# Kernel optimization log

Measured on AMD Instinct MI355X. Metric: run time of the kernel, lower is better.

Reference implementation:

```python
import jax, jax.numpy as jnp
import numpy as np

C, S, K, SIGMA = 512, 11, 3, 16
B = 128
EPS = 1e-5  # BatchNorm eps (eval mode, running_mean=0, running_var=1)


def _make_dct_weight(Cc, H, W):
    # FcaNet 'low16' frequency selection
    lx = [0, 0, 1, 1, 0, 2, 2, 1, 2, 0, 3, 4, 0, 1, 3, 0]
    ly = [0, 1, 0, 1, 2, 0, 1, 2, 2, 3, 0, 0, 4, 3, 1, 5]
    mx = [u * (H // 7) for u in lx]
    my = [v * (W // 7) for v in ly]
    w = np.zeros((Cc, H, W), np.float32)
    cp = Cc // len(lx)

    def bf(pos, freq, POS):
        r = np.cos(np.pi * freq * (pos + 0.5) / POS) / np.sqrt(POS)
        return r if freq == 0 else r * np.sqrt(2.0)

    for i, (u, v) in enumerate(zip(mx, my)):
        for tx in range(H):
            for ty in range(W):
                w[i * cp:(i + 1) * cp, tx, ty] = bf(tx, u, H) * bf(ty, v, W)
    return jnp.asarray(w)


def _bn(f, g, b):
    # eval-mode BatchNorm2d: (f - 0)/sqrt(1+eps)*g + b, per channel (axis 1)
    s = g / jnp.sqrt(1.0 + EPS)
    return f * s[None, :, None, None] + b[None, :, None, None]


def _conv1x1(f, w, b):
    return jnp.einsum('bchw,oc->bohw', f, w) + b[None, :, None, None]


def _spatial_kernel(f, w_conv, b_conv, g_sp, b_sp):
    Bn = f.shape[0]
    s = _conv1x1(f, w_conv, b_conv)                  # (B, K*K, S, S)
    s = s.reshape(Bn, K * K, S * S).transpose(0, 2, 1)  # (B, S*S, K*K)
    s = _bn(s.reshape(Bn, S * S, K, K), g_sp, b_sp)
    return s.reshape(Bn, S * S, K * K)


def _channel_kernel(f, dct_w, fc1, fc2, g_ch, b_ch):
    y = jnp.sum(f * dct_w[None], axis=(-2, -1))      # (B, C) DCT pooling
    y = jax.nn.sigmoid(jax.nn.relu(y @ fc1.T) @ fc2.T)  # (B, C*K*K)
    y = _bn(y.reshape(-1, C, K, K), g_ch, b_ch)
    return y.reshape(-1, C, K * K)


def _unfold(f):
    # torch-style per-pixel kxk neighborhoods -> (B, C, H, W, K, K)
    p = (K + 1) // 2 - 1
    Bn, Cn, H, W = f.shape
    fp = jnp.pad(f, ((0, 0), (0, 0), (p, p), (p, p)))
    pat = jnp.stack([fp[:, :, di:di + H, dj:dj + W]
                     for di in range(K) for dj in range(K)], axis=-1)
    return pat.reshape(Bn, Cn, H, W, K, K)


def setup_inputs() -> dict:
    key = jax.random.key(0)
    ks = iter(jax.random.split(key, 32))

    def nrm(shape, s=0.02):
        return s * jax.random.normal(next(ks), shape, jnp.float32)

    def gma(shape):
        return 1.0 + 0.1 * jax.random.normal(next(ks), shape, jnp.float32)

    return dict(
        x=jax.random.normal(next(ks), (B, C, S, S), jnp.float32),
        dct_w=_make_dct_weight(C, S, S),
        w_conv=nrm((K * K, C)), b_conv=nrm((K * K,)),
        g_sp=gma((S * S,)), b_sp=nrm((S * S,), 0.05),
        g_ch=gma((C,)), b_ch=nrm((C,), 0.05),
        fc1=nrm((C // SIGMA, C)), fc2=nrm((C * K * K, C // SIGMA)),
        up_w1=nrm((2 * C, C)), up_b1=nrm((2 * C,)), up_g1=gma((2 * C,)), up_bb1=nrm((2 * C,), 0.05),
        up_w2=nrm((2 * C, 2 * C)), up_b2=nrm((2 * C,)), up_g2=gma((2 * C,)), up_bb2=nrm((2 * C,), 0.05),
        lo_w1=nrm((2 * C, 2 * C)), lo_b1=nrm((2 * C,)), lo_g1=gma((2 * C,)), lo_bb1=nrm((2 * C,), 0.05),
        lo_w2=nrm((C, 2 * C)), lo_b2=nrm((C,)), lo_g2=gma((C,)), lo_bb2=nrm((C,), 0.05),
    )


def reference(x, dct_w, w_conv, b_conv, g_sp, b_sp, g_ch, b_ch, fc1, fc2,
              up_w1, up_b1, up_g1, up_bb1, up_w2, up_b2, up_g2, up_bb2,
              lo_w1, lo_b1, lo_g1, lo_bb1, lo_w2, lo_b2, lo_g2, lo_bb2):
    Bn = x.shape[0]
    # instance kernel: spatial (B,1,HW,KK) x channel (B,C,1,KK)
    sk = _spatial_kernel(x, w_conv, b_conv, g_sp, b_sp)[:, None]
    ck = _channel_kernel(x, dct_w, fc1, fc2, g_ch, b_ch)[:, :, None]
    inst = (sk * ck).reshape(Bn, C, S, S, K, K)
    # CLM task representation (sum over batch between upper and lower)
    a = jax.nn.relu(_bn(_conv1x1(x, up_w1, up_b1), up_g1, up_bb1))
    a = jax.nn.relu(_bn(_conv1x1(a, up_w2, up_b2), up_g2, up_bb2))
    a = a.sum(axis=0, keepdims=True)
    a = jax.nn.relu(_bn(_conv1x1(a, lo_w1, lo_b1), lo_g1, lo_bb1))
    task_s = jax.nn.sigmoid(_bn(_conv1x1(a, lo_w2, lo_b2), lo_g2, lo_bb2))
    # task kernel (shared across the batch)
    sk_t = _spatial_kernel(task_s, w_conv, b_conv, g_sp, b_sp)[:, None]
    ck_t = _channel_kernel(task_s, dct_w, fc1, fc2, g_ch, b_ch)[:, :, None]
    task_kernel = (sk_t * ck_t).reshape(1, C, S, S, K, K)
    kernel = task_kernel * inst
    adapted = (_unfold(x) * kernel).mean(axis=(-1, -2))  # (B,C,S,S)
    return adapted + x, task_kernel
```

## Files before the change

kernel.cpp:

```cpp
#include <hip/hip_runtime.h>
#include <hip/hip_bf16.h>
#include <math.h>

#define BNEPS 1e-5f
#define BDIM_B 128
#define CDIM 512
#define SS 121
#define KK 9
#define MROWS (BDIM_B * SS)

typedef unsigned short u16;
typedef __bf16 bf16x8 __attribute__((ext_vector_type(8)));
typedef float f32x4 __attribute__((ext_vector_type(4)));

__device__ __forceinline__ u16 f2bf(float f) {
    union { float f; unsigned int u; } v; v.f = f;
    unsigned int r = v.u + 0x7FFF + ((v.u >> 16) & 1);
    return (u16)(r >> 16);
}
__device__ __forceinline__ float bf2f(u16 v) {
    union { unsigned int u; float f; } x; x.u = ((unsigned int)v) << 16; return x.f;
}

__device__ __forceinline__ void gld16(const u16* g, u16* l) {
    __builtin_amdgcn_global_load_lds(
        (const __attribute__((address_space(1))) void*)g,
        (__attribute__((address_space(3))) void*)l, 16, 0, 0);
}

template<int MODE, int SWIZ>
__global__ __launch_bounds__(256)
void gemm_mfma(const u16* __restrict__ A, const u16* __restrict__ Bw,
               const float* __restrict__ bias, const float* __restrict__ g,
               const float* __restrict__ bb, void* __restrict__ out,
               int Kd, int N, int NT)
{
    __shared__ __align__(16) u16 Als[2][128 * 32];
    __shared__ __align__(16) u16 Bls[2][128 * 32];

    const int tid  = threadIdx.x;
    const int lane = tid & 63;
    const int w    = tid >> 6;
    const int wm   = w >> 1, wn = w & 1;

    int bx, by;
    if (SWIZ) {
        int i = blockIdx.x;
        if (i < 960) {
            int xg = i & 7;
            int j  = i >> 3;
            bx = xg * 15 + (j >> 3);
            by = j & 7;
        } else { bx = 120; by = i - 960; }
    } else {
        bx = blockIdx.x / NT; by = blockIdx.x - bx * NT;
    }
    const int bm = bx * 128;
    const int bn = by * 128;

    f32x4 acc[4][4] = {};

    const int subrow = tid >> 2;
    const int kq     = tid & 3;
    const int gchunk = kq ^ ((subrow >> 1) & 3);
    const u16* Ab = A  + (size_t)(bm + subrow) * Kd + gchunk * 8;
    const u16* Bb = Bw + (size_t)(bn + subrow) * Kd + gchunk * 8;
    u16* Al0  = &Als[0][(w * 16) * 32];
    u16* Al1  = &Als[0][(w * 16 + 64) * 32];
    u16* Bl0  = &Bls[0][(w * 16) * 32];
    u16* Bl1  = &Bls[0][(w * 16 + 64) * 32];
    u16* Al0b = &Als[1][(w * 16) * 32];
    u16* Al1b = &Als[1][(w * 16 + 64) * 32];
    u16* Bl0b = &Bls[1][(w * 16) * 32];
    u16* Bl1b = &Bls[1][(w * 16 + 64) * 32];

    const int fa_row = wm * 64 + (lane & 15);
    const int fb_row = wn * 64 + (lane & 15);
    const int kofs   = (((lane >> 4) ^ (((lane & 15) >> 1) & 3))) * 8;

    for (int k0 = 0; k0 < Kd; k0 += 64) {
        __syncthreads();
        gld16(Ab + k0,                      Al0);
        gld16(Ab + (size_t)64 * Kd + k0,    Al1);
        gld16(Bb + k0,                      Bl0);
        gld16(Bb + (size_t)64 * Kd + k0,    Bl1);
        gld16(Ab + k0 + 32,                 Al0b);
        gld16(Ab + (size_t)64 * Kd + k0 + 32, Al1b);
        gld16(Bb + k0 + 32,                 Bl0b);
        gld16(Bb + (size_t)64 * Kd + k0 + 32, Bl1b);
        __syncthreads();

        #pragma unroll
        for (int hb = 0; hb < 2; ++hb) {
            const u16* Ah = &Als[hb][0];
            const u16* Bh = &Bls[hb][0];
            bf16x8 af[4], bfv[4];
            #pragma unroll
            for (int i = 0; i < 4; ++i)
                af[i] = *(const bf16x8*)&Ah[(fa_row + i * 16) * 32 + kofs];
            #pragma unroll
            for (int j = 0; j < 4; ++j)
                bfv[j] = *(const bf16x8*)&Bh[(fb_row + j * 16) * 32 + kofs];
            #pragma unroll
            for (int i = 0; i < 4; ++i)
                #pragma unroll
                for (int j = 0; j < 4; ++j)
                    acc[i][j] = __builtin_amdgcn_mfma_f32_16x16x32_bf16(af[i], bfv[j], acc[i][j], 0, 0, 0);
        }
    }

    const float inv = 1.0f / sqrtf(1.0f + BNEPS);

    if (MODE == 1) {
        u16* Y = (u16*)out;
        int dstrow[4][4];
        #pragma unroll
        for (int i = 0; i < 4; ++i) {
            int mb = bm + wm * 64 + i * 16 + (lane >> 4) * 4;
            #pragma unroll
            for (int r = 0; r < 4; ++r) {
                int m = mb + r;
                int b = m / 121, p = m - b * 121;
                dstrow[i][r] = p * 128 + b;
            }
        }
        #pragma unroll
        for (int j = 0; j < 4; ++j) {
            int n = bn + wn * 64 + j * 16 + (lane & 15);
            float sc = g[n] * inv, bo = bias[n], bv = bb[n];
            #pragma unroll
            for (int i = 0; i < 4; ++i)
                #pragma unroll
                for (int r = 0; r < 4; ++r) {
                    float v = (acc[i][j][r] + bo) * sc + bv;
                    v = fmaxf(v, 0.0f);
                    Y[(size_t)dstrow[i][r] * N + n] = f2bf(v);
                }
        }
    } else if (MODE == 2) {
        float ps[4];
        #pragma unroll
        for (int j = 0; j < 4; ++j) {
            int n = bn + wn * 64 + j * 16 + (lane & 15);
            float sc = g[n] * inv, bo = bias[n], bv = bb[n];
            float s = 0.f;
            #pragma unroll
            for (int i = 0; i < 4; ++i)
                #pragma unroll
                for (int r = 0; r < 4; ++r) {
                    float v = (acc[i][j][r] + bo) * sc + bv;
                    s += fmaxf(v, 0.0f);
                }
            ps[j] = s;
        }
        __syncthreads();
        float* red = (float*)Als;
        #pragma unroll
        for (int j = 0; j < 4; ++j)
            red[(wm * 4 + (lane >> 4)) * 128 + wn * 64 + j * 16 + (lane & 15)] = ps[j];
        __syncthreads();
        if (tid < 128) {
            float s = 0.f;
            #pragma unroll
            for (int r = 0; r < 8; ++r) s += red[r * 128 + tid];
            ((u16*)out)[(size_t)bx * N + bn + tid] = f2bf(s);
        }
    } else {
        u16* Y = (u16*)out;
        #pragma unroll
        for (int j = 0; j < 4; ++j) {
            int n = bn + wn * 64 + j * 16 + (lane & 15);
            float sc = g[n] * inv, bo = bias[n], bv = bb[n];
            #pragma unroll
            for (int i = 0; i < 4; ++i) {
                int mb = bm + wm * 64 + i * 16 + (lane >> 4) * 4;
                #pragma unroll
                for (int r = 0; r < 4; ++r) {
                    float v = (acc[i][j][r] + bo) * sc + bv;
                    if (MODE == 3) v = fmaxf(v, 0.0f);
                    else           v = 1.f / (1.f + expf(-v));
                    Y[(size_t)(mb + r) * N + n] = f2bf(v);
                }
            }
        }
    }
}

#define W1N (1024 * 512)
#define W2N (1024 * 1024)
#define L1N (1024 * 1024)
#define L2N (512 * 1024)
#define DCTN (512 * 121)
#define WCN (16 * 512)
#define PREP_ELEM (W1N + W2N + L1N + L2N + DCTN + WCN)
#define PREP_BLKS (1024 + (PREP_ELEM + 255) / 256)
__global__ void prep_combo(const float* __restrict__ x, u16* __restrict__ Xb,
                           const float* __restrict__ w1, const float* __restrict__ w2,
                           const float* __restrict__ l1, const float* __restrict__ l2,
                           const float* __restrict__ dct, const float* __restrict__ w_conv,
                           u16* __restrict__ o1, u16* __restrict__ o2,
                           u16* __restrict__ o3, u16* __restrict__ o4,
                           float* __restrict__ dctT, u16* __restrict__ wcb)
{
    __shared__ float t[64 * 121];
    if (blockIdx.x < 1024) {
        int b = blockIdx.x >> 3, c0 = (blockIdx.x & 7) * 64;
        for (int idx = threadIdx.x; idx < 64 * 121; idx += 256) {
            int c = idx / 121, p = idx - c * 121;
            t[idx] = x[((size_t)b * 512 + c0 + c) * 121 + p];
        }
        __syncthreads();
        for (int idx = threadIdx.x; idx < 121 * 64; idx += 256) {
            int p = idx >> 6, c = idx & 63;
            Xb[((size_t)(b * 121 + p)) * 512 + c0 + c] = f2bf(t[c * 121 + p]);
        }
        return;
    }
    int i = (blockIdx.x - 1024) * 256 + threadIdx.x;
    if (i < W1N) { o1[i] = f2bf(w1[i]); return; }
    i -= W1N;
    if (i < W2N) { o2[i] = f2bf(w2[i]); return; }
    i -= W2N;
    if (i < L1N) { o3[i] = f2bf(l1[i]); return; }
    i -= L1N;
    if (i < L2N) { o4[i] = f2bf(l2[i]); return; }
    i -= L2N;
    if (i < DCTN) {
        int p = i >> 9, c = i & 511;
        dctT[i] = dct[(size_t)c * 121 + p];
        return;
    }
    i -= DCTN;
    if (i < WCN) {
        int n = i >> 9, c = i & 511;
        wcb[i] = (n < 9) ? f2bf(w_conv[(size_t)n * 512 + c]) : (u16)0;
    }
}

__global__ __launch_bounds__(256)
void spatial_ck_combo(const u16* __restrict__ Xb, const u16* __restrict__ Xt,
                      const u16* __restrict__ wcb, const float* __restrict__ b_conv,
                      const float* __restrict__ g_sp, const float* __restrict__ b_sp,
                      const float* __restrict__ dctT,
                      const float* __restrict__ fc1, const float* __restrict__ fc2,
                      const float* __restrict__ g_ch, const float* __restrict__ b_ch,
                      float* __restrict__ skb, float* __restrict__ skt,
                      float* __restrict__ ckbuf, float* __restrict__ ck_t)
{
    const float inv = 1.0f / sqrtf(1.0f + BNEPS);

    if (blockIdx.x < 122) {
        const int tid  = threadIdx.x;
        const int lane = tid & 63;
        const int w    = tid >> 6;
        const bool task = (blockIdx.x == 121);
        const u16* Arow = task ? Xt : Xb + (size_t)blockIdx.x * 128 * 512;

        const int fr = lane & 15;
        const int kq = lane >> 4;
        const int r0 = w * 32;

        f32x4 acc0 = {}, acc1 = {};
        const u16* a0p = Arow + (size_t)(r0 + fr) * 512 + kq * 8;
        const u16* a1p = Arow + (size_t)(r0 + 16 + fr) * 512 + kq * 8;
        const u16* bp  = wcb + (size_t)fr * 512 + kq * 8;
        #pragma unroll
        for (int k0 = 0; k0 < 512; k0 += 32) {
            bf16x8 a0 = *(const bf16x8*)(a0p + k0);
            bf16x8 a1 = *(const bf16x8*)(a1p + k0);
            bf16x8 b  = *(const bf16x8*)(bp + k0);
            acc0 = __builtin_amdgcn_mfma_f32_16x16x32_bf16(a0, b, acc0, 0, 0, 0);
            acc1 = __builtin_amdgcn_mfma_f32_16x16x32_bf16(a1, b, acc1, 0, 0, 0);
        }

        int n = lane & 15;
        if (n < 9) {
            float bo = b_conv[n];
            #pragma unroll
            for (int t = 0; t < 2; ++t) {
                f32x4 a = t ? acc1 : acc0;
                #pragma unroll
                for (int r = 0; r < 4; ++r) {
                    int mloc = r0 + t * 16 + (lane >> 4) * 4 + r;
                    if (!task) {
                        int m = blockIdx.x * 128 + mloc;
                        int p = m % 121;
                        float v = (a[r] + bo) * (g_sp[p] * inv) + b_sp[p];
                        skb[(size_t)m * 9 + n] = v;
                    } else if (mloc < 121) {
                        float v = (a[r] + bo) * (g_sp[mloc] * inv) + b_sp[mloc];
                        skt[(size_t)mloc * 9 + n] = v;
                    }
                }
            }
        }
        return;
    }

    __shared__ float yls[512];
    __shared__ float y2ls[32];
    const int g = blockIdx.x - 122;
    const u16* src = (g < 128) ? Xb + (size_t)g * 121 * 512 : Xt;

    for (int c = threadIdx.x; c < 512; c += 256) {
        float s = 0.f;
        for (int p = 0; p < SS; ++p)
            s += bf2f(src[(size_t)p * 512 + c]) * dctT[p * 512 + c];
        yls[c] = s;
    }
    __syncthreads();

    {
        int o = threadIdx.x >> 3, kp = threadIdx.x & 7;
        const float* w = fc1 + (size_t)o * 512;
        float s = 0.f;
        for (int k = kp * 4; k < 512; k += 32) {
            float4 wv = *(const float4*)(w + k);
            float4 av = *(const float4*)(yls + k);
            s += wv.x * av.x + wv.y * av.y + wv.z * av.z + wv.w * av.w;
        }
        s += __shfl_xor(s, 1);
        s += __shfl_xor(s, 2);
        s += __shfl_xor(s, 4);
        if (kp == 0) y2ls[o] = fmaxf(s, 0.f);
    }
    __syncthreads();

    for (int o = threadIdx.x; o < CDIM * KK; o += 256) {
        const float* w = fc2 + (size_t)o * 32;
        float s = 0.f;
        #pragma unroll
        for (int k = 0; k < 32; ++k) s += y2ls[k] * w[k];
        s = 1.f / (1.f + expf(-s));
        int c = o / KK;
        s = s * (g_ch[c] * inv) + b_ch[c];
        if (g < 128) ckbuf[(size_t)g * CDIM * KK + o] = s;
        else         ck_t[o] = s;
    }
}

#define TKN (CDIM * SS * KK)
#define FIN_BLKS (1024 + (TKN + 255) / 256)
__global__ __launch_bounds__(256)
void final_combo(const float* __restrict__ x, const float* __restrict__ skb,
                 const float* __restrict__ sk_t, const float* __restrict__ ckbuf,
                 const float* __restrict__ ck_t, float* __restrict__ out0,
                 float* __restrict__ tk)
{
    __shared__ float PS[SS * KK];
    __shared__ float CS[64 * KK];
    __shared__ float XT[64 * SS];

    if (blockIdx.x >= 1024) {
        int idx = (blockIdx.x - 1024) * 256 + threadIdx.x;
        if (idx < TKN) {
            int k9 = idx % KK;
            int pc = idx / KK;
            int p = pc % SS, c = pc / SS;
            tk[idx] = sk_t[p * KK + k9] * ck_t[c * KK + k9];
        }
        return;
    }

    const int tid = threadIdx.x;
    const int b = blockIdx.x >> 3, c0 = (blockIdx.x & 7) * 64;

    const float* sp = skb + (size_t)b * SS * KK;
    for (int i = tid; i < SS * KK; i += 256) PS[i] = sp[i] * sk_t[i];
    const float* cp = ckbuf + ((size_t)b * CDIM + c0) * KK;
    const float* tp = ck_t + (size_t)c0 * KK;
    for (int i = tid; i < 64 * KK; i += 256) CS[i] = cp[i] * tp[i];
    const float* xp = x + ((size_t)b * CDIM + c0) * SS;
    for (int i = tid; i < 64 * SS; i += 256) XT[i] = xp[i];
    __syncthreads();

    float* op = out0 + ((size_t)b * CDIM + c0) * SS;
    for (int i = tid; i < 64 * SS; i += 256) {
        int c = i / SS, p = i - c * SS;
        int h = p / 11, w = p - h * 11;
        const float* xc = XT + c * SS;
        const float* ps = PS + p * KK;
        const float* cs = CS + c * KK;
        float acc = 0.f;
        #pragma unroll
        for (int di = 0; di < 3; ++di) {
            int hh = h + di - 1;
            bool hv = (unsigned)hh < 11u;
            #pragma unroll
            for (int dj = 0; dj < 3; ++dj) {
                int ww = w + dj - 1;
                int k = di * 3 + dj;
                float xv = (hv && (unsigned)ww < 11u) ? xc[hh * 11 + ww] : 0.f;
                acc += xv * ps[k] * cs[k];
            }
        }
        op[i] = acc * (1.0f / 9.0f) + xc[p];
    }
}

extern "C" void kernel_launch(void* const* d_in, const int* in_sizes, int n_in,
                              void* d_out, int out_size, void* d_ws, size_t ws_size,
                              hipStream_t stream)
{
    const float* x      = (const float*)d_in[0];
    const float* dct_w  = (const float*)d_in[1];
    const float* w_conv = (const float*)d_in[2];
    const float* b_conv = (const float*)d_in[3];
    const float* g_sp   = (const float*)d_in[4];
    const float* b_sp   = (const float*)d_in[5];
    const float* g_ch   = (const float*)d_in[6];
    const float* b_ch   = (const float*)d_in[7];
    const float* fc1    = (const float*)d_in[8];
    const float* fc2    = (const float*)d_in[9];
    const float* up_w1  = (const float*)d_in[10];
    const float* up_b1  = (const float*)d_in[11];
    const float* up_g1  = (const float*)d_in[12];
    const float* up_bb1 = (const float*)d_in[13];
    const float* up_w2  = (const float*)d_in[14];
    const float* up_b2  = (const float*)d_in[15];
    const float* up_g2  = (const float*)d_in[16];
    const float* up_bb2 = (const float*)d_in[17];
    const float* lo_w1  = (const float*)d_in[18];
    const float* lo_b1  = (const float*)d_in[19];
    const float* lo_g1  = (const float*)d_in[20];
    const float* lo_bb1 = (const float*)d_in[21];
    const float* lo_w2  = (const float*)d_in[22];
    const float* lo_b2  = (const float*)d_in[23];
    const float* lo_g2  = (const float*)d_in[24];
    const float* lo_bb2 = (const float*)d_in[25];

    float* out0 = (float*)d_out;
    float* tk   = out0 + (size_t)BDIM_B * CDIM * SS;

    char* ws = (char*)d_ws;
    size_t off = 0;
    auto alloc = [&](size_t bytes) { void* p = ws + off; off += (bytes + 63) & ~(size_t)63; return p; };
    u16*   Xb      = (u16*)alloc((size_t)MROWS * 512 * 2);
    u16*   Y1      = (u16*)alloc((size_t)MROWS * 1024 * 2);
    u16*   w1b     = (u16*)alloc((size_t)W1N * 2);
    u16*   w2b     = (u16*)alloc((size_t)W2N * 2);
    u16*   lw1b    = (u16*)alloc((size_t)L1N * 2);
    u16*   lw2b    = (u16*)alloc((size_t)L2N * 2);
    u16*   asum_b  = (u16*)alloc((size_t)128 * 1024 * 2);
    u16*   a3b     = (u16*)alloc((size_t)128 * 1024 * 2);
    u16*   ts_pc   = (u16*)alloc((size_t)128 * 512 * 2);
    float* dctT    = (float*)alloc((size_t)SS * 512 * 4);
    u16*   wcb     = (u16*)alloc((size_t)WCN * 2);
    float* ckbuf   = (float*)alloc((size_t)BDIM_B * CDIM * KK * 4);
    float* skbuf   = (float*)alloc((size_t)BDIM_B * SS * KK * 4);
    float* ck_t    = (float*)alloc((size_t)CDIM * KK * 4);
    float* sk_t    = (float*)alloc((size_t)SS * KK * 4);

    hipLaunchKernelGGL(prep_combo, dim3(PREP_BLKS), dim3(256), 0, stream,
                       x, Xb, up_w1, up_w2, lo_w1, lo_w2, dct_w, w_conv,
                       w1b, w2b, lw1b, lw2b, dctT, wcb);

    hipLaunchKernelGGL((gemm_mfma<1, 1>), dim3(121 * 8), dim3(256), 0, stream,
                       Xb, w1b, up_b1, up_g1, up_bb1, (void*)Y1, 512, 1024, 8);
    hipLaunchKernelGGL((gemm_mfma<2, 1>), dim3(121 * 8), dim3(256), 0, stream,
                       Y1, w2b, up_b2, up_g2, up_bb2, (void*)asum_b, 1024, 1024, 8);

    hipLaunchKernelGGL((gemm_mfma<3, 0>), dim3(8), dim3(256), 0, stream,
                       asum_b, lw1b, lo_b1, lo_g1, lo_bb1, (void*)a3b, 1024, 1024, 8);
    hipLaunchKernelGGL((gemm_mfma<4, 0>), dim3(4), dim3(256), 0, stream,
                       a3b, lw2b, lo_b2, lo_g2, lo_bb2, (void*)ts_pc, 1024, 512, 4);

    hipLaunchKernelGGL(spatial_ck_combo, dim3(122 + 129), dim3(256), 0, stream,
                       Xb, ts_pc, wcb, b_conv, g_sp, b_sp,
                       dctT, fc1, fc2, g_ch, b_ch,
                       skbuf, sk_t, ckbuf, ck_t);

    hipLaunchKernelGGL(final_combo, dim3(FIN_BLKS), dim3(256), 0, stream,
                       x, skbuf, sk_t, ckbuf, ck_t, out0, tk);
}
```

Baseline: 318.3 us.

## Double-buffer GEMM K-loop, fuse small GEMMs with spatial/channel kernels, vectorize loads

The main MFMA GEMM loop now uses a double-buffered LDS scheme. It prefetches the next 32-wide K slice while computing the current one, with one barrier per step instead of two. The small lower-branch GEMMs move to a new direct-load MFMA kernel. The first of them is fused into one launch with the per-instance spatial and channel kernel work, and the task-kernel computation is split into its own tiny launch. Weight bf16 conversion, channel-kernel DCT pooling, and the final epilogue loads and stores are vectorized, trading some code complexity for fewer launches and better overlap.

```diff
diff --git a/kernel.cpp b/kernel.cpp
--- a/kernel.cpp
+++ b/kernel.cpp
@@ -65,49 +65,41 @@
     const int gchunk = kq ^ ((subrow >> 1) & 3);
     const u16* Ab = A  + (size_t)(bm + subrow) * Kd + gchunk * 8;
     const u16* Bb = Bw + (size_t)(bn + subrow) * Kd + gchunk * 8;
-    u16* Al0  = &Als[0][(w * 16) * 32];
-    u16* Al1  = &Als[0][(w * 16 + 64) * 32];
-    u16* Bl0  = &Bls[0][(w * 16) * 32];
-    u16* Bl1  = &Bls[0][(w * 16 + 64) * 32];
-    u16* Al0b = &Als[1][(w * 16) * 32];
-    u16* Al1b = &Als[1][(w * 16 + 64) * 32];
-    u16* Bl0b = &Bls[1][(w * 16) * 32];
-    u16* Bl1b = &Bls[1][(w * 16 + 64) * 32];
 
     const int fa_row = wm * 64 + (lane & 15);
     const int fb_row = wn * 64 + (lane & 15);
     const int kofs   = (((lane >> 4) ^ (((lane & 15) >> 1) & 3))) * 8;
 
-    for (int k0 = 0; k0 < Kd; k0 += 64) {
+    const int NK = Kd >> 5;
+
+#define STG(bf_, t_) do { \
+    gld16(Ab + (size_t)(t_) * 32,                 &Als[bf_][(w * 16) * 32]); \
+    gld16(Ab + (size_t)64 * Kd + (size_t)(t_) * 32, &Als[bf_][(w * 16 + 64) * 32]); \
+    gld16(Bb + (size_t)(t_) * 32,                 &Bls[bf_][(w * 16) * 32]); \
+    gld16(Bb + (size_t)64 * Kd + (size_t)(t_) * 32, &Bls[bf_][(w * 16 + 64) * 32]); \
+} while (0)
+
+    STG(0, 0);
+    __syncthreads();
+    int cur = 0;
+    for (int t = 0; t < NK; ++t) {
+        if (t + 1 < NK) STG(cur ^ 1, t + 1);
+        bf16x8 af[4], bfv[4];
+        #pragma unroll
+        for (int i = 0; i < 4; ++i)
+            af[i] = *(const bf16x8*)&Als[cur][(fa_row + i * 16) * 32 + kofs];
+        #pragma unroll
+        for (int j = 0; j < 4; ++j)
+            bfv[j] = *(const bf16x8*)&Bls[cur][(fb_row + j * 16) * 32 + kofs];
+        #pragma unroll
+        for (int i = 0; i < 4; ++i)
+            #pragma unroll
+            for (int j = 0; j < 4; ++j)
+                acc[i][j] = __builtin_amdgcn_mfma_f32_16x16x32_bf16(af[i], bfv[j], acc[i][j], 0, 0, 0);
         __syncthreads();
-        gld16(Ab + k0,                      Al0);
-        gld16(Ab + (size_t)64 * Kd + k0,    Al1);
-        gld16(Bb + k0,                      Bl0);
-        gld16(Bb + (size_t)64 * Kd + k0,    Bl1);
-        gld16(Ab + k0 + 32,                 Al0b);
-        gld16(Ab + (size_t)64 * Kd + k0 + 32, Al1b);
-        gld16(Bb + k0 + 32,                 Bl0b);
-        gld16(Bb + (size_t)64 * Kd + k0 + 32, Bl1b);
-        __syncthreads();
-
-        #pragma unroll
-        for (int hb = 0; hb < 2; ++hb) {
-            const u16* Ah = &Als[hb][0];
-            const u16* Bh = &Bls[hb][0];
-            bf16x8 af[4], bfv[4];
-            #pragma unroll
-            for (int i = 0; i < 4; ++i)
-                af[i] = *(const bf16x8*)&Ah[(fa_row + i * 16) * 32 + kofs];
-            #pragma unroll
-            for (int j = 0; j < 4; ++j)
-                bfv[j] = *(const bf16x8*)&Bh[(fb_row + j * 16) * 32 + kofs];
-            #pragma unroll
-            for (int i = 0; i < 4; ++i)
-                #pragma unroll
-                for (int j = 0; j < 4; ++j)
-                    acc[i][j] = __builtin_amdgcn_mfma_f32_16x16x32_bf16(af[i], bfv[j], acc[i][j], 0, 0, 0);
-        }
-    }
+        cur ^= 1;
+    }
+#undef STG
 
     const float inv = 1.0f / sqrtf(1.0f + BNEPS);
 
@@ -137,7 +129,7 @@
                     Y[(size_t)dstrow[i][r] * N + n] = f2bf(v);
                 }
         }
-    } else if (MODE == 2) {
+    } else {
         float ps[4];
         #pragma unroll
         for (int j = 0; j < 4; ++j) {
@@ -165,34 +157,217 @@
             for (int r = 0; r < 8; ++r) s += red[r * 128 + tid];
             ((u16*)out)[(size_t)bx * N + bn + tid] = f2bf(s);
         }
-    } else {
-        u16* Y = (u16*)out;
+    }
+}
+
+template<int MODE>
+__device__ __forceinline__ void gemm_small_body(
+    const u16* __restrict__ A, const u16* __restrict__ Bw,
+    const float* __restrict__ bias, const float* __restrict__ g,
+    const float* __restrict__ bb, u16* __restrict__ Y,
+    int Kd, int N, int bn)
+{
+    const int tid  = threadIdx.x;
+    const int lane = tid & 63;
+    const int w    = tid >> 6;
+    const int fr   = lane & 15;
+    const int kq   = lane >> 4;
+    const int r0   = w * 32;
+
+    f32x4 acc[2][4] = {};
+    const u16* a0p = A + (size_t)(r0 + fr) * Kd + kq * 8;
+    const u16* a1p = a0p + (size_t)16 * Kd;
+    const u16* bp  = Bw + (size_t)(bn + fr) * Kd + kq * 8;
+
+    #pragma unroll 4
+    for (int k0 = 0; k0 < Kd; k0 += 32) {
+        bf16x8 a0 = *(const bf16x8*)(a0p + k0);
+        bf16x8 a1 = *(const bf16x8*)(a1p + k0);
         #pragma unroll
         for (int j = 0; j < 4; ++j) {
-            int n = bn + wn * 64 + j * 16 + (lane & 15);
-            float sc = g[n] * inv, bo = bias[n], bv = bb[n];
-            #pragma unroll
-            for (int i = 0; i < 4; ++i) {
-                int mb = bm + wm * 64 + i * 16 + (lane >> 4) * 4;
-                #pragma unroll
-                for (int r = 0; r < 4; ++r) {
-                    float v = (acc[i][j][r] + bo) * sc + bv;
-                    if (MODE == 3) v = fmaxf(v, 0.0f);
-                    else           v = 1.f / (1.f + expf(-v));
-                    Y[(size_t)(mb + r) * N + n] = f2bf(v);
+            bf16x8 bv = *(const bf16x8*)(bp + (size_t)j * 16 * Kd + k0);
+            acc[0][j] = __builtin_amdgcn_mfma_f32_16x16x32_bf16(a0, bv, acc[0][j], 0, 0, 0);
+            acc[1][j] = __builtin_amdgcn_mfma_f32_16x16x32_bf16(a1, bv, acc[1][j], 0, 0, 0);
+        }
+    }
+
+    const float inv = 1.0f / sqrtf(1.0f + BNEPS);
+    #pragma unroll
+    for (int j = 0; j < 4; ++j) {
+        int n = bn + j * 16 + (lane & 15);
+        float sc = g[n] * inv, bo = bias[n], bv = bb[n];
+        #pragma unroll
+        for (int t = 0; t < 2; ++t)
+            #pragma unroll
+            for (int r = 0; r < 4; ++r) {
+                int m = r0 + t * 16 + (lane >> 4) * 4 + r;
+                float v = (acc[t][j][r] + bo) * sc + bv;
+                if (MODE == 3) v = fmaxf(v, 0.0f);
+                else           v = 1.f / (1.f + expf(-v));
+                Y[(size_t)m * N + n] = f2bf(v);
+            }
+    }
+}
+
+template<int MODE>
+__global__ __launch_bounds__(256)
+void gemm_small(const u16* __restrict__ A, const u16* __restrict__ Bw,
+                const float* __restrict__ bias, const float* __restrict__ g,
+                const float* __restrict__ bb, u16* __restrict__ Y,
+                int Kd, int N)
+{
+    gemm_small_body<MODE>(A, Bw, bias, g, bb, Y, Kd, N, blockIdx.x * 64);
+}
+
+__device__ __forceinline__ void spatial_body(
+    const u16* __restrict__ Arow, const u16* __restrict__ wcb,
+    const float* __restrict__ b_conv, const float* __restrict__ g_sp,
+    const float* __restrict__ b_sp, float* __restrict__ skb,
+    bool task, int blk, float* __restrict__ skt)
+{
+    const float inv = 1.0f / sqrtf(1.0f + BNEPS);
+    const int tid  = threadIdx.x;
+    const int lane = tid & 63;
+    const int w    = tid >> 6;
+    const int fr   = lane & 15;
+    const int kq   = lane >> 4;
+    const int r0   = w * 32;
+
+    f32x4 acc0 = {}, acc1 = {};
+    const u16* a0p = Arow + (size_t)(r0 + fr) * 512 + kq * 8;
+    const u16* a1p = a0p + (size_t)16 * 512;
+    const u16* bp  = wcb + (size_t)fr * 512 + kq * 8;
+    #pragma unroll
+    for (int k0 = 0; k0 < 512; k0 += 32) {
+        bf16x8 a0 = *(const bf16x8*)(a0p + k0);
+        bf16x8 a1 = *(const bf16x8*)(a1p + k0);
+        bf16x8 b  = *(const bf16x8*)(bp + k0);
+        acc0 = __builtin_amdgcn_mfma_f32_16x16x32_bf16(a0, b, acc0, 0, 0, 0);
+        acc1 = __builtin_amdgcn_mfma_f32_16x16x32_bf16(a1, b, acc1, 0, 0, 0);
+    }
+
+    int n = lane & 15;
+    if (n < 9) {
+        float bo = b_conv[n];
+        #pragma unroll
+        for (int t = 0; t < 2; ++t) {
+            f32x4 a = t ? acc1 : acc0;
+            #pragma unroll
+            for (int r = 0; r < 4; ++r) {
+                int mloc = r0 + t * 16 + (lane >> 4) * 4 + r;
+                if (!task) {
+                    int m = blk * 128 + mloc;
+                    int p = m % 121;
+                    float v = (a[r] + bo) * (g_sp[p] * inv) + b_sp[p];
+                    skb[(size_t)m * 9 + n] = v;
+                } else if (mloc < 121) {
+                    float v = (a[r] + bo) * (g_sp[mloc] * inv) + b_sp[mloc];
+                    skt[(size_t)mloc * 9 + n] = v;
                 }
             }
         }
     }
+}
+
+__device__ __forceinline__ void channel_body(
+    const u16* __restrict__ src, const float* __restrict__ dctT,
+    const float* __restrict__ fc1, const float* __restrict__ fc2,
+    const float* __restrict__ g_ch, const float* __restrict__ b_ch,
+    float* __restrict__ outp, float* yls, float* y2ls)
+{
+    const float inv = 1.0f / sqrtf(1.0f + BNEPS);
+
+    {
+        int c = threadIdx.x * 2;
+        float s0 = 0.f, s1 = 0.f;
+        for (int p = 0; p < SS; ++p) {
+            unsigned v = *(const unsigned*)(src + (size_t)p * 512 + c);
+            float2 d  = *(const float2*)(dctT + (size_t)p * 512 + c);
+            s0 += bf2f((u16)(v & 0xFFFFu)) * d.x;
+            s1 += bf2f((u16)(v >> 16)) * d.y;
+        }
+        yls[c] = s0; yls[c + 1] = s1;
+    }
+    __syncthreads();
+
+    {
+        int o = threadIdx.x >> 3, kp = threadIdx.x & 7;
+        const float* w = fc1 + (size_t)o * 512;
+        float s = 0.f;
+        for (int k = kp * 4; k < 512; k += 32) {
+            float4 wv = *(const float4*)(w + k);
+            float4 av = *(const float4*)(yls + k);
+            s += wv.x * av.x + wv.y * av.y + wv.z * av.z + wv.w * av.w;
+        }
+        s += __shfl_xor(s, 1);
+        s += __shfl_xor(s, 2);
+        s += __shfl_xor(s, 4);
+        if (kp == 0) y2ls[o] = fmaxf(s, 0.f);
+    }
+    __syncthreads();
+
+    for (int o = threadIdx.x; o < CDIM * KK; o += 256) {
+        const float* w = fc2 + (size_t)o * 32;
+        float s = 0.f;
+        #pragma unroll
+        for (int k = 0; k < 32; ++k) s += y2ls[k] * w[k];
+        s = 1.f / (1.f + expf(-s));
+        int c = o / KK;
+        s = s * (g_ch[c] * inv) + b_ch[c];
+        outp[o] = s;
+    }
+}
+
+__global__ __launch_bounds__(256)
+void lo1_spatial(const u16* __restrict__ asum_b, const u16* __restrict__ lw1b,
+                 const float* __restrict__ lo_b1, const float* __restrict__ lo_g1,
+                 const float* __restrict__ lo_bb1, u16* __restrict__ a3b,
+                 const u16* __restrict__ Xb, const u16* __restrict__ wcb,
+                 const float* __restrict__ b_conv, const float* __restrict__ g_sp,
+                 const float* __restrict__ b_sp, const float* __restrict__ dctT,
+                 const float* __restrict__ fc1, const float* __restrict__ fc2,
+                 const float* __restrict__ g_ch, const float* __restrict__ b_ch,
+                 float* __restrict__ skb, float* __restrict__ ckbuf)
+{
+    __shared__ float sm[544];
+    int bi = blockIdx.x;
+    if (bi < 16) {
+        gemm_small_body<3>(asum_b, lw1b, lo_b1, lo_g1, lo_bb1, a3b, 1024, 1024, bi * 64);
+        return;
+    }
+    bi -= 16;
+    if (bi < 121) {
+        spatial_body(Xb + (size_t)bi * 128 * 512, wcb, b_conv, g_sp, b_sp, skb, false, bi, nullptr);
+        return;
+    }
+    bi -= 121;
+    channel_body(Xb + (size_t)bi * 121 * 512, dctT, fc1, fc2, g_ch, b_ch,
+                 ckbuf + (size_t)bi * CDIM * KK, sm, sm + 512);
+}
+
+__global__ __launch_bounds__(256)
+void task_combo(const u16* __restrict__ ts_pc, const u16* __restrict__ wcb,
+                const float* __restrict__ b_conv, const float* __restrict__ g_sp,
+                const float* __restrict__ b_sp, const float* __restrict__ dctT,
+                const float* __restrict__ fc1, const float* __restrict__ fc2,
+                const float* __restrict__ g_ch, const float* __restrict__ b_ch,
+                float* __restrict__ skt, float* __restrict__ ck_t)
+{
+    __shared__ float sm[544];
+    if (blockIdx.x == 0)
+        spatial_body(ts_pc, wcb, b_conv, g_sp, b_sp, nullptr, true, 0, skt);
+    else
+        channel_body(ts_pc, dctT, fc1, fc2, g_ch, b_ch, ck_t, sm, sm + 512);
 }
 
 #define W1N (1024 * 512)
 #define W2N (1024 * 1024)
 #define L1N (1024 * 1024)
 #define L2N (512 * 1024)
+#define VECN ((W1N + W2N + L1N + L2N) / 4)
 #define DCTN (512 * 121)
 #define WCN (16 * 512)
-#define PREP_ELEM (W1N + W2N + L1N + L2N + DCTN + WCN)
+#define PREP_ELEM (VECN + DCTN + WCN)
 #define PREP_BLKS (1024 + (PREP_ELEM + 255) / 256)
 __global__ void prep_combo(const float* __restrict__ x, u16* __restrict__ Xb,
                            const float* __restrict__ w1, const float* __restrict__ w2,
@@ -217,14 +392,21 @@
         return;
     }
     int i = (blockIdx.x - 1024) * 256 + threadIdx.x;
-    if (i < W1N) { o1[i] = f2bf(w1[i]); return; }
-    i -= W1N;
-    if (i < W2N) { o2[i] = f2bf(w2[i]); return; }
-    i -= W2N;
-    if (i < L1N) { o3[i] = f2bf(l1[i]); return; }
-    i -= L1N;
-    if (i < L2N) { o4[i] = f2bf(l2[i]); return; }
-    i -= L2N;
+    if (i < VECN) {
+        int q = i;
+        const float* s; u16* d;
+        if (q < W1N / 4)                    { s = w1; d = o1; }
+        else if (q < (W1N + W2N) / 4)       { s = w2; d = o2; q -= W1N / 4; }
+        else if (q < (W1N + W2N + L1N) / 4) { s = l1; d = o3; q -= (W1N + W2N) / 4; }
+        else                                { s = l2; d = o4; q -= (W1N + W2N + L1N) / 4; }
+        float4 v = ((const float4*)s)[q];
+        uint2 r;
+        r.x = (unsigned)f2bf(v.x) | ((unsigned)f2bf(v.y) << 16);
+        r.y = (unsigned)f2bf(v.z) | ((unsigned)f2bf(v.w) << 16);
+        ((uint2*)d)[q] = r;
+        return;
+    }
+    i -= VECN;
     if (i < DCTN) {
         int p = i >> 9, c = i & 511;
         dctT[i] = dct[(size_t)c * 121 + p];
@@ -234,108 +416,6 @@
     if (i < WCN) {
         int n = i >> 9, c = i & 511;
         wcb[i] = (n < 9) ? f2bf(w_conv[(size_t)n * 512 + c]) : (u16)0;
-    }
-}
-
-__global__ __launch_bounds__(256)
-void spatial_ck_combo(const u16* __restrict__ Xb, const u16* __restrict__ Xt,
-                      const u16* __restrict__ wcb, const float* __restrict__ b_conv,
-                      const float* __restrict__ g_sp, const float* __restrict__ b_sp,
-                      const float* __restrict__ dctT,
-                      const float* __restrict__ fc1, const float* __restrict__ fc2,
-                      const float* __restrict__ g_ch, const float* __restrict__ b_ch,
-                      float* __restrict__ skb, float* __restrict__ skt,
-                      float* __restrict__ ckbuf, float* __restrict__ ck_t)
-{
-    const float inv = 1.0f / sqrtf(1.0f + BNEPS);
-
-    if (blockIdx.x < 122) {
-        const int tid  = threadIdx.x;
-        const int lane = tid & 63;
-        const int w    = tid >> 6;
-        const bool task = (blockIdx.x == 121);
-        const u16* Arow = task ? Xt : Xb + (size_t)blockIdx.x * 128 * 512;
-
-        const int fr = lane & 15;
-        const int kq = lane >> 4;
-        const int r0 = w * 32;
-
-        f32x4 acc0 = {}, acc1 = {};
-        const u16* a0p = Arow + (size_t)(r0 + fr) * 512 + kq * 8;
-        const u16* a1p = Arow + (size_t)(r0 + 16 + fr) * 512 + kq * 8;
-        const u16* bp  = wcb + (size_t)fr * 512 + kq * 8;
-        #pragma unroll
-        for (int k0 = 0; k0 < 512; k0 += 32) {
-            bf16x8 a0 = *(const bf16x8*)(a0p + k0);
-            bf16x8 a1 = *(const bf16x8*)(a1p + k0);
-            bf16x8 b  = *(const bf16x8*)(bp + k0);
-            acc0 = __builtin_amdgcn_mfma_f32_16x16x32_bf16(a0, b, acc0, 0, 0, 0);
-            acc1 = __builtin_amdgcn_mfma_f32_16x16x32_bf16(a1, b, acc1, 0, 0, 0);
-        }
-
-        int n = lane & 15;
-        if (n < 9) {
-            float bo = b_conv[n];
-            #pragma unroll
-            for (int t = 0; t < 2; ++t) {
-                f32x4 a = t ? acc1 : acc0;
-                #pragma unroll
-                for (int r = 0; r < 4; ++r) {
-                    int mloc = r0 + t * 16 + (lane >> 4) * 4 + r;
-                    if (!task) {
-                        int m = blockIdx.x * 128 + mloc;
-                        int p = m % 121;
-                        float v = (a[r] + bo) * (g_sp[p] * inv) + b_sp[p];
-                        skb[(size_t)m * 9 + n] = v;
-                    } else if (mloc < 121) {
-                        float v = (a[r] + bo) * (g_sp[mloc] * inv) + b_sp[mloc];
-                        skt[(size_t)mloc * 9 + n] = v;
-                    }
-                }
-            }
-        }
-        return;
-    }
-
-    __shared__ float yls[512];
-    __shared__ float y2ls[32];
-    const int g = blockIdx.x - 122;
-    const u16* src = (g < 128) ? Xb + (size_t)g * 121 * 512 : Xt;
-
-    for (int c = threadIdx.x; c < 512; c += 256) {
-        float s = 0.f;
-        for (int p = 0; p < SS; ++p)
-            s += bf2f(src[(size_t)p * 512 + c]) * dctT[p * 512 + c];
-        yls[c] = s;
-    }
-    __syncthreads();
-
-    {
-        int o = threadIdx.x >> 3, kp = threadIdx.x & 7;
-        const float* w = fc1 + (size_t)o * 512;
-        float s = 0.f;
-        for (int k = kp * 4; k < 512; k += 32) {
-            float4 wv = *(const float4*)(w + k);
-            float4 av = *(const float4*)(yls + k);
-            s += wv.x * av.x + wv.y * av.y + wv.z * av.z + wv.w * av.w;
-        }
-        s += __shfl_xor(s, 1);
-        s += __shfl_xor(s, 2);
-        s += __shfl_xor(s, 4);
-        if (kp == 0) y2ls[o] = fmaxf(s, 0.f);
-    }
-    __syncthreads();
-
-    for (int o = threadIdx.x; o < CDIM * KK; o += 256) {
-        const float* w = fc2 + (size_t)o * 32;
-        float s = 0.f;
-        #pragma unroll
-        for (int k = 0; k < 32; ++k) s += y2ls[k] * w[k];
-        s = 1.f / (1.f + expf(-s));
-        int c = o / KK;
-        s = s * (g_ch[c] * inv) + b_ch[c];
-        if (g < 128) ckbuf[(size_t)g * CDIM * KK + o] = s;
-        else         ck_t[o] = s;
     }
 }
 
@@ -369,32 +449,44 @@
     for (int i = tid; i < SS * KK; i += 256) PS[i] = sp[i] * sk_t[i];
     const float* cp = ckbuf + ((size_t)b * CDIM + c0) * KK;
     const float* tp = ck_t + (size_t)c0 * KK;
-    for (int i = tid; i < 64 * KK; i += 256) CS[i] = cp[i] * tp[i];
+    for (int i = tid; i < (64 * KK) / 4; i += 256) {
+        float4 a = ((const float4*)cp)[i];
+        float4 bq = ((const float4*)tp)[i];
+        float4 r; r.x = a.x * bq.x; r.y = a.y * bq.y; r.z = a.z * bq.z; r.w = a.w * bq.w;
+        ((float4*)CS)[i] = r;
+    }
     const float* xp = x + ((size_t)b * CDIM + c0) * SS;
-    for (int i = tid; i < 64 * SS; i += 256) XT[i] = xp[i];
+    for (int i = tid; i < (64 * SS) / 4; i += 256)
+        ((float4*)XT)[i] = ((const float4*)xp)[i];
     __syncthreads();
 
     float* op = out0 + ((size_t)b * CDIM + c0) * SS;
-    for (int i = tid; i < 64 * SS; i += 256) {
-        int c = i / SS, p = i - c * SS;
-        int h = p / 11, w = p - h * 11;
-        const float* xc = XT + c * SS;
-        const float* ps = PS + p * KK;
-        const float* cs = CS + c * KK;
-        float acc = 0.f;
-        #pragma unroll
-        for (int di = 0; di < 3; ++di) {
-            int hh = h + di - 1;
-            bool hv = (unsigned)hh < 11u;
-            #pragma unroll
-            for (int dj = 0; dj < 3; ++dj) {
-                int ww = w + dj - 1;
-                int k = di * 3 + dj;
-                float xv = (hv && (unsigned)ww < 11u) ? xc[hh * 11 + ww] : 0.f;
-                acc += xv * ps[k] * cs[k];
+    for (int ci = tid; ci < (64 * SS) / 4; ci += 256) {
+        float4 o;
+        #pragma unroll
+        for (int r = 0; r < 4; ++r) {
+            int i = ci * 4 + r;
+            int c = i / SS, p = i - c * SS;
+            int h = p / 11, w = p - h * 11;
+            const float* xc = XT + c * SS;
+            const float* ps = PS + p * KK;
+            const float* cs = CS + c * KK;
+            float acc = 0.f;
+            #pragma unroll
+            for (int di = 0; di < 3; ++di) {
+                int hh = h + di - 1;
+                bool hv = (unsigned)hh < 11u;
+                #pragma unroll
+                for (int dj = 0; dj < 3; ++dj) {
+                    int ww = w + dj - 1;
+                    int k = di * 3 + dj;
+                    float xv = (hv && (unsigned)ww < 11u) ? xc[hh * 11 + ww] : 0.f;
+                    acc += xv * ps[k] * cs[k];
+                }
             }
-        }
-        op[i] = acc * (1.0f / 9.0f) + xc[p];
+            ((float*)&o)[r] = acc * (1.0f / 9.0f) + xc[p];
+        }
+        ((float4*)op)[ci] = o;
     }
 }
 
@@ -460,15 +552,18 @@
     hipLaunchKernelGGL((gemm_mfma<2, 1>), dim3(121 * 8), dim3(256), 0, stream,
                        Y1, w2b, up_b2, up_g2, up_bb2, (void*)asum_b, 1024, 1024, 8);
 
-    hipLaunchKernelGGL((gemm_mfma<3, 0>), dim3(8), dim3(256), 0, stream,
-                       asum_b, lw1b, lo_b1, lo_g1, lo_bb1, (void*)a3b, 1024, 1024, 8);
-    hipLaunchKernelGGL((gemm_mfma<4, 0>), dim3(4), dim3(256), 0, stream,
-                       a3b, lw2b, lo_b2, lo_g2, lo_bb2, (void*)ts_pc, 1024, 512, 4);
-
-    hipLaunchKernelGGL(spatial_ck_combo, dim3(122 + 129), dim3(256), 0, stream,
-                       Xb, ts_pc, wcb, b_conv, g_sp, b_sp,
+    hipLaunchKernelGGL(lo1_spatial, dim3(16 + 121 + 128), dim3(256), 0, stream,
+                       asum_b, lw1b, lo_b1, lo_g1, lo_bb1, a3b,
+                       Xb, wcb, b_conv, g_sp, b_sp,
                        dctT, fc1, fc2, g_ch, b_ch,
-                       skbuf, sk_t, ckbuf, ck_t);
+                       skbuf, ckbuf);
+
+    hipLaunchKernelGGL((gemm_small<4>), dim3(8), dim3(256), 0, stream,
+                       a3b, lw2b, lo_b2, lo_g2, lo_bb2, ts_pc, 1024, 512);
+
+    hipLaunchKernelGGL(task_combo, dim3(2), dim3(256), 0, stream,
+                       ts_pc, wcb, b_conv, g_sp, b_sp,
+                       dctT, fc1, fc2, g_ch, b_ch, sk_t, ck_t);
 
     hipLaunchKernelGGL(final_combo, dim3(FIN_BLKS), dim3(256), 0, stream,
                        x, skbuf, sk_t, ckbuf, ck_t, out0, tk);
```

Result: slower. 349.7 us (+9.8%).
